# Performance work log

Measured on AMD Instinct MI355X. Metric: run time of the kernel, lower is better.

Reference implementation:

```python
import jax, jax.numpy as jnp
import numpy as np

N, C_IN, C_OUT = 8192, 256, 128
NEG_SLOPE = 0.2


def setup_inputs() -> dict:
    key = jax.random.key(0)
    k0, k1, k2, k3, k4 = jax.random.split(key, 5)
    x = jax.random.normal(k0, (N, C_IN), dtype=jnp.float32)
    # sparse-ish binary dense adjacency, avg degree ~32
    adj = (jax.random.uniform(k1, (N, N)) < (32.0 / N)).astype(jnp.float32)
    W = jax.random.normal(k2, (C_IN, C_OUT), dtype=jnp.float32) * 0.05
    att_src = jax.random.normal(k3, (C_OUT,), dtype=jnp.float32) * 0.1
    att_dst = jax.random.normal(k4, (C_OUT,), dtype=jnp.float32) * 0.1
    bias = jnp.zeros((C_OUT,), dtype=jnp.float32)
    return {"x": x, "adj": adj, "W": W, "att_src": att_src,
            "att_dst": att_dst, "bias": bias}


def reference(x, adj, W, att_src, att_dst, bias):
    n = adj.shape[0]
    idx = jnp.arange(n)
    adj = adj.at[idx, idx].set(1.0)          # add self loops
    h = x @ W                                 # [N, C_out]
    a_src = h @ att_src                       # [N]
    a_dst = h @ att_dst                       # [N]
    alpha = a_src[:, None] + a_dst[None, :]   # [N, N]
    alpha = jax.nn.leaky_relu(alpha, NEG_SLOPE)
    alpha = adj * jnp.exp(alpha)              # masked exp
    alpha = alpha / alpha.sum(axis=0, keepdims=True)  # column-normalize (dim=0)
    out = (adj * alpha).T @ h + bias          # [N, C_out]
    return out
```

## Files before the change

kernel.cpp:

```cpp
#include <hip/hip_runtime.h>
#include <hip/hip_bf16.h>

#define NN 8192
#define CIN 256
#define COUT 128
#define GR 32
#define GKT 64
#define CH 8
#define ICH (NN / CH)
#define KT 64
#define HTS 72

typedef unsigned short u16;
typedef _Float16 f16;
typedef __attribute__((ext_vector_type(8))) short short8;
typedef __attribute__((ext_vector_type(8))) _Float16 f16x8;
typedef __attribute__((ext_vector_type(16))) float f32x16;

__device__ __forceinline__ short8 pack8_bf16(const float* v) {
    union { __hip_bfloat162 b2[4]; short8 s; } u;
    #pragma unroll
    for (int q = 0; q < 4; ++q)
        u.b2[q] = __float22bfloat162_rn(make_float2(v[2 * q], v[2 * q + 1]));
    return u.s;
}

__device__ __forceinline__ void load_lds16(const float* g, float* l) {
    __builtin_amdgcn_global_load_lds(
        (const __attribute__((address_space(1))) void*)g,
        (__attribute__((address_space(3))) void*)l, 16, 0, 0);
}

__global__ __launch_bounds__(256) void gemm_h(const float* __restrict__ x,
                                              const float* __restrict__ W,
                                              const float* __restrict__ att_src,
                                              const float* __restrict__ att_dst,
                                              u16* __restrict__ h_t,
                                              float* __restrict__ a_src,
                                              float* __restrict__ a_dst) {
    __shared__ float Wt[GKT * COUT];
    __shared__ float xt[GKT][GR + 4];
    __shared__ float ot[GR][COUT + 4];
    int tid = threadIdx.x;
    int i0 = blockIdx.x * GR;
    int tx = tid & 31, ty = tid >> 5;
    int c0 = tx * 4, r0 = ty * 4;
    int xr = tid >> 3, xk = (tid & 7) * 8;
    float acc[4][4] = {};

    for (int kt = 0; kt < CIN; kt += GKT) {
        float4 wv[8];
        #pragma unroll
        for (int j = 0; j < 8; ++j) {
            int f = j * 256 + tid;
            wv[j] = *(const float4*)&W[(size_t)(kt + (f >> 5)) * COUT + (f & 31) * 4];
        }
        float4 xv0 = *(const float4*)&x[(size_t)(i0 + xr) * CIN + kt + xk];
        float4 xv1 = *(const float4*)&x[(size_t)(i0 + xr) * CIN + kt + xk + 4];
        __syncthreads();
        #pragma unroll
        for (int j = 0; j < 8; ++j)
            *(float4*)&Wt[(j * 256 + tid) * 4] = wv[j];
        xt[xk + 0][xr] = xv0.x; xt[xk + 1][xr] = xv0.y;
        xt[xk + 2][xr] = xv0.z; xt[xk + 3][xr] = xv0.w;
        xt[xk + 4][xr] = xv1.x; xt[xk + 5][xr] = xv1.y;
        xt[xk + 6][xr] = xv1.z; xt[xk + 7][xr] = xv1.w;
        __syncthreads();
        #pragma unroll 8
        for (int k = 0; k < GKT; ++k) {
            float4 wk = *(const float4*)&Wt[k * COUT + c0];
            float4 xf = *(const float4*)&xt[k][r0];
            float xa[4] = {xf.x, xf.y, xf.z, xf.w};
            #pragma unroll
            for (int a = 0; a < 4; ++a) {
                acc[a][0] += xa[a] * wk.x; acc[a][1] += xa[a] * wk.y;
                acc[a][2] += xa[a] * wk.z; acc[a][3] += xa[a] * wk.w;
            }
        }
    }

    float4 asv = *(const float4*)&att_src[c0];
    float4 adv = *(const float4*)&att_dst[c0];
    #pragma unroll
    for (int a = 0; a < 4; ++a) {
        float4 o = make_float4(acc[a][0], acc[a][1], acc[a][2], acc[a][3]);
        *(float4*)&ot[r0 + a][c0] = o;
        float s = o.x * asv.x + o.y * asv.y + o.z * asv.z + o.w * asv.w;
        float d = o.x * adv.x + o.y * adv.y + o.z * adv.z + o.w * adv.w;
        #pragma unroll
        for (int m = 16; m >= 1; m >>= 1) {
            s += __shfl_xor(s, m, 32);
            d += __shfl_xor(d, m, 32);
        }
        if (tx == 0) {
            a_src[i0 + r0 + a] = s;
            a_dst[i0 + r0 + a] = d;
        }
    }
    __syncthreads();
    int c = tid >> 1, hf = tid & 1;
    float vals[16];
    #pragma unroll
    for (int q = 0; q < 16; ++q) vals[q] = ot[hf * 16 + q][c];
    *(short8*)(h_t + (size_t)c * NN + i0 + hf * 16)     = pack8_bf16(vals);
    *(short8*)(h_t + (size_t)c * NN + i0 + hf * 16 + 8) = pack8_bf16(vals + 8);
}

__global__ __launch_bounds__(256) void gat_mm(const float* __restrict__ adj,
                                              const u16* __restrict__ h_t,
                                              const float* __restrict__ a_src,
                                              const float* __restrict__ a_dst,
                                              f16* __restrict__ pout,
                                              float* __restrict__ pden) {
    __shared__ float tileA[KT * COUT];
    __shared__ u16 htS[128 * HTS];
    __shared__ float asrcS[ICH];
    int tid = threadIdx.x;
    int lane = tid & 63, w = tid >> 6;
    int jb = blockIdx.x & 63, ch = blockIdx.x >> 6;
    int j0 = jb * 128;
    int i0 = ch * ICH;
    int half = lane >> 5;
    int jloc = w * 32 + (lane & 31);
    int gj = j0 + jloc;
    float dj = a_dst[gj];

    ((float4*)asrcS)[tid] = ((const float4*)(a_src + i0))[tid];

    f32x16 acc[4];
    #pragma unroll
    for (int nt = 0; nt < 4; ++nt)
        #pragma unroll
        for (int q = 0; q < 16; ++q) acc[nt][q] = 0.f;
    float dsum = 0.f;
    __syncthreads();

    for (int s = 0; s < ICH / KT; ++s) {
        int ib = i0 + s * KT;
        #pragma unroll
        for (int q = 0; q < 8; ++q) {
            int f = q * 256 + tid;
            const float* gp = adj + (size_t)(ib + (f >> 5)) * NN + j0 + (f & 31) * 4;
            load_lds16(gp, &tileA[f * 4]);
        }
        short8 bv[4];
        int bc[4], bi[4];
        #pragma unroll
        for (int q = 0; q < 4; ++q) {
            int p = q * 256 + tid;
            bc[q] = p >> 3; bi[q] = (p & 7) * 8;
            bv[q] = *(const short8*)(h_t + (size_t)bc[q] * NN + ib + bi[q]);
        }
        #pragma unroll
        for (int q = 0; q < 4; ++q)
            *(short8*)(htS + bc[q] * HTS + bi[q]) = bv[q];
        __syncthreads();

        #pragma unroll
        for (int kk = 0; kk < 4; ++kk) {
            int kb = kk * 16 + half * 8;
            int gib = ib + kb;
            short8 bf[4];
            #pragma unroll
            for (int nt = 0; nt < 4; ++nt) {
                int c = nt * 32 + (lane & 31);
                bf[nt] = *(const short8*)(htS + c * HTS + kb);
            }
            float av[8];
            #pragma unroll
            for (int e = 0; e < 8; ++e)
                av[e] = tileA[(kb + e) * COUT + jloc];
            float4 s0 = *(const float4*)&asrcS[s * KT + kb];
            float4 s1 = *(const float4*)&asrcS[s * KT + kb + 4];
            float sv[8] = {s0.x, s0.y, s0.z, s0.w, s1.x, s1.y, s1.z, s1.w};
            float pv[8];
            #pragma unroll
            for (int e = 0; e < 8; ++e) {
                float t = sv[e] + dj;
                float ev = __expf(fmaxf(t, 0.2f * t));
                int gi = gib + e;
                pv[e] = (av[e] != 0.f || gi == gj) ? ev : 0.f;
                dsum += pv[e];
            }
            short8 af = pack8_bf16(pv);
            #pragma unroll
            for (int nt = 0; nt < 4; ++nt)
                acc[nt] = __builtin_amdgcn_mfma_f32_32x32x16_bf16(af, bf[nt],
                                                                  acc[nt], 0, 0, 0);
        }
        __syncthreads();
    }

    #pragma unroll
    for (int nt = 0; nt < 4; ++nt) {
        int c = nt * 32 + (lane & 31);
        #pragma unroll
        for (int r = 0; r < 16; ++r) {
            int row = (r & 3) + 8 * (r >> 2) + 4 * half;
            int j = j0 + w * 32 + row;
            pout[((size_t)ch * NN + j) * COUT + c] = (f16)acc[nt][r];
        }
    }
    float dall = dsum + __shfl_xor(dsum, 32, 64);
    if (half == 0) pden[(size_t)ch * NN + gj] = dall;
}

__global__ __launch_bounds__(256) void gat_reduce(const f16* __restrict__ pout,
                                                  const float* __restrict__ pden,
                                                  const float* __restrict__ bias,
                                                  float* __restrict__ out) {
    int idx = blockIdx.x * 256 + threadIdx.x;
    int j = idx >> 4;
    int c8 = (idx & 15) * 8;
    f16x8 pv[CH];
    #pragma unroll
    for (int ch = 0; ch < CH; ++ch)
        pv[ch] = *(const f16x8*)(pout + ((size_t)ch * NN + j) * COUT + c8);
    float den = 0.f;
    #pragma unroll
    for (int ch = 0; ch < CH; ++ch) den += pden[(size_t)ch * NN + j];
    float s[8] = {};
    #pragma unroll
    for (int ch = 0; ch < CH; ++ch)
        #pragma unroll
        for (int q = 0; q < 8; ++q) s[q] += (float)pv[ch][q];
    float inv = 1.0f / den;
    float4 b0 = *(const float4*)&bias[c8];
    float4 b1 = *(const float4*)&bias[c8 + 4];
    float4 o0 = make_float4(s[0] * inv + b0.x, s[1] * inv + b0.y,
                            s[2] * inv + b0.z, s[3] * inv + b0.w);
    float4 o1 = make_float4(s[4] * inv + b1.x, s[5] * inv + b1.y,
                            s[6] * inv + b1.z, s[7] * inv + b1.w);
    *(float4*)&out[(size_t)j * COUT + c8]     = o0;
    *(float4*)&out[(size_t)j * COUT + c8 + 4] = o1;
}

extern "C" void kernel_launch(void* const* d_in, const int* in_sizes, int n_in,
                              void* d_out, int out_size, void* d_ws, size_t ws_size,
                              hipStream_t stream) {
    const float* x       = (const float*)d_in[0];
    const float* adj     = (const float*)d_in[1];
    const float* W       = (const float*)d_in[2];
    const float* att_src = (const float*)d_in[3];
    const float* att_dst = (const float*)d_in[4];
    const float* bias    = (const float*)d_in[5];
    float* out = (float*)d_out;

    u16*   h_t   = (u16*)d_ws;
    float* a_src = (float*)((char*)d_ws + (size_t)2 * 1024 * 1024);
    float* a_dst = a_src + NN;
    float* pden  = a_dst + NN;
    f16*   pout  = (f16*)(pden + (size_t)CH * NN);

    gemm_h    <<<NN / GR, 256, 0, stream>>>(x, W, att_src, att_dst, h_t, a_src, a_dst);
    gat_mm    <<<64 * CH, 256, 0, stream>>>(adj, h_t, a_src, a_dst, pout, pden);
    gat_reduce<<<NN * COUT / 8 / 256, 256, 0, stream>>>(pout, pden, bias, out);
}
```

Baseline: 398.2 us.

## Compress adjacency tiles to LDS bitmasks via ballot and double the i-chunk split

The adjacency tile is now loaded into registers and turned into per-row bitmasks with wave ballots, so it no longer goes to LDS through async global_load_lds. This shrinks the 32KB float LDS tile to a 1KB mask, and with launch_bounds(256,3) it aims for higher occupancy. The row split doubles from 8 to 16 chunks, which gives more blocks. The price is a larger partial-output buffer and more work in the reduce kernel, plus extra register pressure and ballot instructions.

```diff
diff --git a/kernel.cpp b/kernel.cpp
--- a/kernel.cpp
+++ b/kernel.cpp
@@ -6,7 +6,7 @@
 #define COUT 128
 #define GR 32
 #define GKT 64
-#define CH 8
+#define CH 16
 #define ICH (NN / CH)
 #define KT 64
 #define HTS 72
@@ -23,12 +23,6 @@
     for (int q = 0; q < 4; ++q)
         u.b2[q] = __float22bfloat162_rn(make_float2(v[2 * q], v[2 * q + 1]));
     return u.s;
-}
-
-__device__ __forceinline__ void load_lds16(const float* g, float* l) {
-    __builtin_amdgcn_global_load_lds(
-        (const __attribute__((address_space(1))) void*)g,
-        (__attribute__((address_space(3))) void*)l, 16, 0, 0);
 }
 
 __global__ __launch_bounds__(256) void gemm_h(const float* __restrict__ x,
@@ -106,13 +100,13 @@
     *(short8*)(h_t + (size_t)c * NN + i0 + hf * 16 + 8) = pack8_bf16(vals + 8);
 }
 
-__global__ __launch_bounds__(256) void gat_mm(const float* __restrict__ adj,
-                                              const u16* __restrict__ h_t,
-                                              const float* __restrict__ a_src,
-                                              const float* __restrict__ a_dst,
-                                              f16* __restrict__ pout,
-                                              float* __restrict__ pden) {
-    __shared__ float tileA[KT * COUT];
+__global__ __launch_bounds__(256, 3) void gat_mm(const float* __restrict__ adj,
+                                                 const u16* __restrict__ h_t,
+                                                 const float* __restrict__ a_src,
+                                                 const float* __restrict__ a_dst,
+                                                 f16* __restrict__ pout,
+                                                 float* __restrict__ pden) {
+    __shared__ unsigned int maskS[KT * 4];
     __shared__ u16 htS[128 * HTS];
     __shared__ float asrcS[ICH];
     int tid = threadIdx.x;
@@ -123,9 +117,11 @@
     int half = lane >> 5;
     int jloc = w * 32 + (lane & 31);
     int gj = j0 + jloc;
+    int slot = lane & 3;
+    int kbit = jloc >> 2;
     float dj = a_dst[gj];
-
-    ((float4*)asrcS)[tid] = ((const float4*)(a_src + i0))[tid];
+    if (tid < ICH / 4)
+        ((float4*)asrcS)[tid] = ((const float4*)(a_src + i0))[tid];
 
     f32x16 acc[4];
     #pragma unroll
@@ -137,14 +133,13 @@
 
     for (int s = 0; s < ICH / KT; ++s) {
         int ib = i0 + s * KT;
+        float4 v[8];
         #pragma unroll
         for (int q = 0; q < 8; ++q) {
             int f = q * 256 + tid;
-            const float* gp = adj + (size_t)(ib + (f >> 5)) * NN + j0 + (f & 31) * 4;
-            load_lds16(gp, &tileA[f * 4]);
-        }
-        short8 bv[4];
-        int bc[4], bi[4];
+            v[q] = *(const float4*)&adj[(size_t)(ib + (f >> 5)) * NN + j0 + (f & 31) * 4];
+        }
+        short8 bv[4]; int bc[4], bi[4];
         #pragma unroll
         for (int q = 0; q < 4; ++q) {
             int p = q * 256 + tid;
@@ -152,6 +147,18 @@
             bv[q] = *(const short8*)(h_t + (size_t)bc[q] * NN + ib + bi[q]);
         }
         #pragma unroll
+        for (int q = 0; q < 8; ++q) {
+            unsigned long long b0 = __ballot(v[q].x != 0.f);
+            unsigned long long b1 = __ballot(v[q].y != 0.f);
+            unsigned long long b2 = __ballot(v[q].z != 0.f);
+            unsigned long long b3 = __ballot(v[q].w != 0.f);
+            unsigned long long bb = slot == 0 ? b0 : slot == 1 ? b1
+                                  : slot == 2 ? b2 : b3;
+            unsigned int mw = (unsigned int)(bb >> (half * 32));
+            int R = q * 8 + w * 2 + half;
+            if ((lane & 31) < 4) maskS[R * 4 + slot] = mw;
+        }
+        #pragma unroll
         for (int q = 0; q < 4; ++q)
             *(short8*)(htS + bc[q] * HTS + bi[q]) = bv[q];
         __syncthreads();
@@ -162,24 +169,16 @@
             int gib = ib + kb;
             short8 bf[4];
             #pragma unroll
-            for (int nt = 0; nt < 4; ++nt) {
-                int c = nt * 32 + (lane & 31);
-                bf[nt] = *(const short8*)(htS + c * HTS + kb);
-            }
-            float av[8];
-            #pragma unroll
-            for (int e = 0; e < 8; ++e)
-                av[e] = tileA[(kb + e) * COUT + jloc];
-            float4 s0 = *(const float4*)&asrcS[s * KT + kb];
-            float4 s1 = *(const float4*)&asrcS[s * KT + kb + 4];
-            float sv[8] = {s0.x, s0.y, s0.z, s0.w, s1.x, s1.y, s1.z, s1.w};
+            for (int nt = 0; nt < 4; ++nt)
+                bf[nt] = *(const short8*)(htS + (nt * 32 + (lane & 31)) * HTS + kb);
             float pv[8];
             #pragma unroll
             for (int e = 0; e < 8; ++e) {
-                float t = sv[e] + dj;
+                unsigned int mw = maskS[(kb + e) * 4 + slot];
+                float t = asrcS[s * KT + kb + e] + dj;
                 float ev = __expf(fmaxf(t, 0.2f * t));
-                int gi = gib + e;
-                pv[e] = (av[e] != 0.f || gi == gj) ? ev : 0.f;
+                bool on = ((mw >> kbit) & 1u) | (gib + e == gj);
+                pv[e] = on ? ev : 0.f;
                 dsum += pv[e];
             }
             short8 af = pack8_bf16(pv);
@@ -212,18 +211,16 @@
     int idx = blockIdx.x * 256 + threadIdx.x;
     int j = idx >> 4;
     int c8 = (idx & 15) * 8;
-    f16x8 pv[CH];
-    #pragma unroll
-    for (int ch = 0; ch < CH; ++ch)
-        pv[ch] = *(const f16x8*)(pout + ((size_t)ch * NN + j) * COUT + c8);
     float den = 0.f;
     #pragma unroll
     for (int ch = 0; ch < CH; ++ch) den += pden[(size_t)ch * NN + j];
     float s[8] = {};
     #pragma unroll
-    for (int ch = 0; ch < CH; ++ch)
-        #pragma unroll
-        for (int q = 0; q < 8; ++q) s[q] += (float)pv[ch][q];
+    for (int ch = 0; ch < CH; ++ch) {
+        f16x8 pv = *(const f16x8*)(pout + ((size_t)ch * NN + j) * COUT + c8);
+        #pragma unroll
+        for (int q = 0; q < 8; ++q) s[q] += (float)pv[q];
+    }
     float inv = 1.0f / den;
     float4 b0 = *(const float4*)&bias[c8];
     float4 b1 = *(const float4*)&bias[c8 + 4];
```

Result: slower. 407.0 us (+2.2%).
